# Kernel optimization log

Measured on AMD Instinct MI355X. Metric: run time of the kernel, lower is better.

Reference implementation:

```python
import jax, jax.numpy as jnp
import numpy as np

N, E, D, H, OUT = 100000, 1600000, 64, 64, 4


def _glorot(key, i, o):
    s = (6.0 / (i + o)) ** 0.5
    return jax.random.uniform(key, (i, o), jnp.float32, -s, s)


def setup_inputs() -> dict:
    key = jax.random.key(0)
    ks = jax.random.split(key, 5)
    x = jax.random.normal(ks[0], (N, D), jnp.float32)
    edge_index = jax.random.randint(ks[1], (2, E), 0, N, jnp.int32)
    return {
        "x": x,
        "edge_index": edge_index,
        "W0": _glorot(ks[2], D, H), "b0": jnp.zeros((H,), jnp.float32),
        "W1": _glorot(ks[3], H, H), "b1": jnp.zeros((H,), jnp.float32),
        "W2": _glorot(ks[4], H, OUT), "b2": jnp.zeros((OUT,), jnp.float32),
    }


def _gcn_layer(x, src, dst, W, b):
    # WeightedGCNConv.forward: remove_self_loops, then gcn_norm with
    # add_self_loops=True (self-loop weight 1), symmetric normalization,
    # scatter-add aggregation, then Linear.
    n = x.shape[0]
    w = (src != dst).astype(x.dtype)           # zero out original self loops
    deg = jax.ops.segment_sum(w, dst, num_segments=n) + 1.0  # +1 from added self loop
    dis = jax.lax.rsqrt(deg)                   # deg >= 1, no inf
    norm = dis[src] * w * dis[dst]             # [E]
    agg = jax.ops.segment_sum(norm[:, None] * x[src], dst, num_segments=n)
    agg = agg + (dis * dis)[:, None] * x       # self-loop contribution
    return agg @ W + b


def reference(x, edge_index, W0, b0, W1, b1, W2, b2):
    src, dst = edge_index[0], edge_index[1]    # flow source_to_target
    # Dropout is identity in eval mode.
    h = jax.nn.relu(_gcn_layer(x, src, dst, W0, b0))
    h = jax.nn.relu(_gcn_layer(h, src, dst, W1, b1))
    return _gcn_layer(h, src, dst, W2, b2)     # [N, 4]
```

## Files before the change

kernel.cpp:

```cpp
#include <hip/hip_runtime.h>
#include <hip/hip_fp16.h>


#define BLK 256
#define NBITS 7
#define NBW   (1 << NBITS)
#define G     8
#define CHUNK 4096
#define EPT   (CHUNK / BLK)
#define CAPG  384
#define PAD   16

__global__ void k_binA(const int* __restrict__ src, const int* __restrict__ dst,
                       int* __restrict__ bcur, int* __restrict__ binned,
                       int E, int nb) {
    __shared__ int lcnt[1024];
    __shared__ int lbase[1024];
    int t = threadIdx.x;
    int g = blockIdx.x & (G - 1);
    for (int i = t; i < nb; i += BLK) lcnt[i] = 0;
    __syncthreads();

    int e0 = blockIdx.x * CHUNK;
    int bs[EPT], vs[EPT];
#pragma unroll
    for (int i = 0; i < EPT; ++i) {
        int e = e0 + i * BLK + t;
        bs[i] = -1;
        if (e < E) {
            int s = src[e], d = dst[e];
            if (s != d) {
                bs[i] = d >> NBITS;
                vs[i] = (s << NBITS) | (d & (NBW - 1));
                atomicAdd(&lcnt[bs[i]], 1);
            }
        }
    }
    __syncthreads();
    for (int i = t; i < nb; i += BLK) {
        int c = lcnt[i];
        lbase[i] = c ? atomicAdd(&bcur[(g * nb + i) * PAD], c) : 0;
    }
    __syncthreads();
    for (int i = t; i < nb; i += BLK) lcnt[i] = 0;
    __syncthreads();
#pragma unroll
    for (int i = 0; i < EPT; ++i) {
        if (bs[i] >= 0) {
            int p = lbase[bs[i]] + atomicAdd(&lcnt[bs[i]], 1);
            if (p < CAPG) binned[(size_t)(g * nb + bs[i]) * CAPG + p] = vs[i];
        }
    }
}

__global__ void k_binB(const int* __restrict__ bcur, const int* __restrict__ binned,
                       int* __restrict__ cursor, int2* __restrict__ rowinfo,
                       float* __restrict__ dis, int* __restrict__ srcs,
                       int n, int nb) {
    __shared__ int cnt[NBW];
    __shared__ int scan[NBW];
    __shared__ int sbase;
    int b = blockIdx.x;
    int t = threadIdx.x;
    if (t < NBW) cnt[t] = 0;
    __syncthreads();
    for (int g = 0; g < G; ++g) {
        int m = min(bcur[(g * nb + b) * PAD], CAPG);
        const int* reg = binned + (size_t)(g * nb + b) * CAPG;
        for (int i = t; i < m; i += BLK)
            atomicAdd(&cnt[reg[i] & (NBW - 1)], 1);
    }
    __syncthreads();
    int c = 0;
    if (t < NBW) { c = cnt[t]; scan[t] = c; }
    __syncthreads();
    for (int off = 1; off < NBW; off <<= 1) {
        int u = (t < NBW && t >= off) ? scan[t - off] : 0;
        __syncthreads();
        if (t < NBW) scan[t] += u;
        __syncthreads();
    }
    if (t == NBW - 1) sbase = atomicAdd(cursor, scan[NBW - 1]);
    __syncthreads();
    int base = sbase;
    if (t < NBW) {
        int excl = scan[t] - c;
        int node = b * NBW + t;
        if (node < n) {
            rowinfo[node] = make_int2(base + excl, c);
            dis[node] = rsqrtf((float)c + 1.0f);
        }
    }
    __syncthreads();
    if (t < NBW) scan[t] = scan[t] - c;
    __syncthreads();
    for (int g = 0; g < G; ++g) {
        int m = min(bcur[(g * nb + b) * PAD], CAPG);
        const int* reg = binned + (size_t)(g * nb + b) * CAPG;
        for (int i = t; i < m; i += BLK) {
            int v = reg[i];
            int p = atomicAdd(&scan[v & (NBW - 1)], 1);
            srcs[base + p] = v >> NBITS;
        }
    }
}

__global__ void k_gemm64(const float* __restrict__ in, const float* __restrict__ W,
                         const float* __restrict__ dis, __half* __restrict__ z16, int n) {
    __shared__ float rows[4][64];
    int c  = threadIdx.x & 63;
    int r4 = threadIdx.x >> 6;
    float Wr[64];
#pragma unroll
    for (int k = 0; k < 64; ++k) Wr[k] = W[k * 64 + c];
    const float4* rp = reinterpret_cast<const float4*>(&rows[r4][0]);
    for (long base = (long)blockIdx.x * 4; base < n; base += (long)gridDim.x * 4) {
        long row = base + r4;
        __syncthreads();
        if (row < n) rows[r4][c] = in[row * 64 + c];
        __syncthreads();
        if (row < n) {
            float acc = 0.0f;
#pragma unroll
            for (int k4 = 0; k4 < 16; ++k4) {
                float4 rv = rp[k4];
                acc = fmaf(rv.x, Wr[4 * k4 + 0], acc);
                acc = fmaf(rv.y, Wr[4 * k4 + 1], acc);
                acc = fmaf(rv.z, Wr[4 * k4 + 2], acc);
                acc = fmaf(rv.w, Wr[4 * k4 + 3], acc);
            }
            z16[row * 64 + c] = __float2half(dis[row] * acc);
        }
    }
}

__device__ __forceinline__ float4 gather_row(const float2* __restrict__ zrow,
                                             const int2* __restrict__ rowinfo,
                                             const int* __restrict__ srcs,
                                             int node, int lane, int p, int hi) {
    float4 acc = make_float4(0.f, 0.f, 0.f, 0.f);
    if (hi == 0) {
        float2 r = zrow[(long)node * 16 + p];
        float2 a = __half22float2(*reinterpret_cast<__half2*>(&r.x));
        float2 bq = __half22float2(*reinterpret_cast<__half2*>(&r.y));
        acc = make_float4(a.x, a.y, bq.x, bq.y);
    }
    int2 ri = rowinfo[node];
    int beg = ri.x, end = ri.x + ri.y;
    for (int base = beg; base < end; base += 64) {
        int m = min(end - base, 64);
        int s = (lane < m) ? srcs[base + lane] : 0;
        int mf = m & ~3;
#pragma unroll 8
        for (int j = 0; j < mf; j += 4) {
            int sj = __shfl(s, j + hi);
            float2 r = zrow[(long)sj * 16 + p];
            float2 a = __half22float2(*reinterpret_cast<__half2*>(&r.x));
            float2 bq = __half22float2(*reinterpret_cast<__half2*>(&r.y));
            acc.x += a.x; acc.y += a.y; acc.z += bq.x; acc.w += bq.y;
        }
        if (m & 3) {
            int idx = mf + hi;
            int sj = __shfl(s, idx < 64 ? idx : 63);
            if (idx < m) {
                float2 r = zrow[(long)sj * 16 + p];
                float2 a = __half22float2(*reinterpret_cast<__half2*>(&r.x));
                float2 bq = __half22float2(*reinterpret_cast<__half2*>(&r.y));
                acc.x += a.x; acc.y += a.y; acc.z += bq.x; acc.w += bq.y;
            }
        }
    }
    acc.x += __shfl_xor(acc.x, 16); acc.y += __shfl_xor(acc.y, 16);
    acc.z += __shfl_xor(acc.z, 16); acc.w += __shfl_xor(acc.w, 16);
    acc.x += __shfl_xor(acc.x, 32); acc.y += __shfl_xor(acc.y, 32);
    acc.z += __shfl_xor(acc.z, 32); acc.w += __shfl_xor(acc.w, 32);
    return acc;
}

__global__ void k_aggW1(const float2* __restrict__ zrow, const int2* __restrict__ rowinfo,
                        const int* __restrict__ srcs, const float* __restrict__ dis,
                        const float* __restrict__ b0, const float* __restrict__ W1,
                        __half* __restrict__ z1, int n) {
    __shared__ __half2 W1t[32 * 64];
    __shared__ float hrow[4][64];
    for (int i = threadIdx.x; i < 32 * 64; i += BLK) {
        int c = i & 63, k2 = i >> 6;
        W1t[i] = __floats2half2_rn(W1[(2 * k2) * 64 + c], W1[(2 * k2 + 1) * 64 + c]);
    }
    __syncthreads();

    int lane = threadIdx.x & 63;
    int wv   = threadIdx.x >> 6;
    int node = blockIdx.x * (BLK / 64) + wv;
    if (node >= n) return;
    int p = lane & 15, hi = lane >> 4;

    float4 acc = gather_row(zrow, rowinfo, srcs, node, lane, p, hi);

    float dd = dis[node];
    float4 bb = reinterpret_cast<const float4*>(b0)[p];
    if (hi == 0) {
        float4 h;
        h.x = fmaxf(dd * acc.x + bb.x, 0.f);
        h.y = fmaxf(dd * acc.y + bb.y, 0.f);
        h.z = fmaxf(dd * acc.z + bb.z, 0.f);
        h.w = fmaxf(dd * acc.w + bb.w, 0.f);
        *reinterpret_cast<float4*>(&hrow[wv][4 * p]) = h;
    }
    asm volatile("s_waitcnt lgkmcnt(0)" ::: "memory");

    const float4* hq = reinterpret_cast<const float4*>(&hrow[wv][0]);
    float o = 0.f;
#pragma unroll
    for (int k4 = 0; k4 < 16; ++k4) {
        float4 hv = hq[k4];
        float2 wa = __half22float2(W1t[(2 * k4 + 0) * 64 + lane]);
        float2 wb = __half22float2(W1t[(2 * k4 + 1) * 64 + lane]);
        o = fmaf(hv.x, wa.x, o);
        o = fmaf(hv.y, wa.y, o);
        o = fmaf(hv.z, wb.x, o);
        o = fmaf(hv.w, wb.y, o);
    }
    z1[(long)node * 64 + lane] = __float2half(dd * o);
}

__global__ void k_aggW2(const float2* __restrict__ zrow, const int2* __restrict__ rowinfo,
                        const int* __restrict__ srcs, const float* __restrict__ dis,
                        const float* __restrict__ b1, const float* __restrict__ W2,
                        float* __restrict__ y2, int n) {
    __shared__ float W2l[64 * 4];
    if (threadIdx.x < 256) W2l[threadIdx.x] = W2[threadIdx.x];
    __syncthreads();
    int lane = threadIdx.x & 63;
    int node = blockIdx.x * (BLK / 64) + (threadIdx.x >> 6);
    if (node >= n) return;
    int p = lane & 15, hi = lane >> 4;

    float4 acc = gather_row(zrow, rowinfo, srcs, node, lane, p, hi);

    float dd = dis[node];
    float4 bb = reinterpret_cast<const float4*>(b1)[p];
    float h0 = fmaxf(dd * acc.x + bb.x, 0.f);
    float h1 = fmaxf(dd * acc.y + bb.y, 0.f);
    float h2 = fmaxf(dd * acc.z + bb.z, 0.f);
    float h3 = fmaxf(dd * acc.w + bb.w, 0.f);
    float pc[4];
#pragma unroll
    for (int c = 0; c < 4; ++c) {
        pc[c] = h0 * W2l[(4 * p + 0) * 4 + c] + h1 * W2l[(4 * p + 1) * 4 + c]
              + h2 * W2l[(4 * p + 2) * 4 + c] + h3 * W2l[(4 * p + 3) * 4 + c];
    }
#pragma unroll
    for (int off = 1; off < 16; off <<= 1) {
#pragma unroll
        for (int c = 0; c < 4; ++c) pc[c] += __shfl_xor(pc[c], off);
    }
    if (lane == 0) {
        reinterpret_cast<float4*>(y2)[node] =
            make_float4(dd * pc[0], dd * pc[1], dd * pc[2], dd * pc[3]);
    }
}

__global__ void k_agg4(const float* __restrict__ z2, const int2* __restrict__ rowinfo,
                       const int* __restrict__ srcs, const float* __restrict__ dis,
                       const float* __restrict__ b, float* __restrict__ out, int n) {
    long t = (long)blockIdx.x * blockDim.x + threadIdx.x;
    int i = (int)(t >> 2), c = (int)(t & 3);
    if (i < n) {
        float acc = z2[(long)i * 4 + c];
        int2 ri = rowinfo[i];
        int beg = ri.x, end = ri.x + ri.y;
        for (int e = beg; e < end; ++e)
            acc += z2[(long)srcs[e] * 4 + c];
        out[(long)i * 4 + c] = dis[i] * acc + b[c];
    }
}

extern "C" void kernel_launch(void* const* d_in, const int* in_sizes, int n_in,
                              void* d_out, int out_size, void* d_ws, size_t ws_size,
                              hipStream_t stream) {
    const float* x  = (const float*)d_in[0];
    const int*   ei = (const int*)d_in[1];
    const float* W0 = (const float*)d_in[2];
    const float* b0 = (const float*)d_in[3];
    const float* W1 = (const float*)d_in[4];
    const float* b1 = (const float*)d_in[5];
    const float* W2 = (const float*)d_in[6];
    const float* b2 = (const float*)d_in[7];
    float* out = (float*)d_out;

    const int n = in_sizes[0] / 64;
    const int E = in_sizes[1] / 2;
    const int* src = ei;
    const int* dst = ei + E;
    const int nb = (n + NBW - 1) / NBW;

    int*    bcur     = (int*)d_ws;
    int*    cursor   = bcur + G * nb * PAD;
    int2*   rowinfo  = (int2*)(cursor + 16);
    int*    srcs     = (int*)(rowinfo + n);
    float*  dis      = (float*)(srcs + E);
    __half* z16      = (__half*)(dis + n);
    __half* z1       = z16 + (size_t)n * 64;
    float*  y2       = (float*)(z1 + (size_t)n * 64);
    int*    binned   = (int*)z1;

    const int gWave  = (n + (BLK / 64) - 1) / (BLK / 64);
    const int gN4    = (int)(((long)n * 4 + BLK - 1) / BLK);
    const int gGemm  = 2048;
    const int nchunk = (E + CHUNK - 1) / CHUNK;

    hipMemsetAsync(bcur, 0, ((size_t)G * nb * PAD + 16) * sizeof(int), stream);
    k_binA<<<nchunk, BLK, 0, stream>>>(src, dst, bcur, binned, E, nb);
    k_binB<<<nb, BLK, 0, stream>>>(bcur, binned, cursor, rowinfo, dis, srcs, n, nb);

    k_gemm64<<<gGemm, BLK, 0, stream>>>(x, W0, dis, z16, n);

    k_aggW1<<<gWave, BLK, 0, stream>>>((const float2*)z16, rowinfo, srcs, dis, b0, W1,
                                       z1, n);

    k_aggW2<<<gWave, BLK, 0, stream>>>((const float2*)z1, rowinfo, srcs, dis, b1, W2,
                                       y2, n);

    k_agg4<<<gN4, BLK, 0, stream>>>(y2, rowinfo, srcs, dis, b2, out, n);
}
```

Before: 248.3 us.

## Unfuse layer-1 transform into separate aggregate and GEMM kernels; reread edges in binning

Splits the fused aggregate+W1 kernel into a pure aggregation kernel that writes the biased fp16 row, followed by a templated GEMM kernel that applies ReLU on load and scales by dis. The binning kernel now streams each chunk twice from global memory instead of holding edges in registers, and the chunk size is doubled. This is meant to cut register pressure and per-wave LDS work in the aggregation kernel. In exchange it adds an extra kernel launch, an extra fp16 round trip of the full hidden activation, and a second read of the edge list during binning.

```diff
diff --git a/kernel.cpp b/kernel.cpp
--- a/kernel.cpp
+++ b/kernel.cpp
@@ -6,8 +6,7 @@
 #define NBITS 7
 #define NBW   (1 << NBITS)
 #define G     8
-#define CHUNK 4096
-#define EPT   (CHUNK / BLK)
+#define CHUNK 8192
 #define CAPG  384
 #define PAD   16
 
@@ -22,33 +21,24 @@
     __syncthreads();
 
     int e0 = blockIdx.x * CHUNK;
-    int bs[EPT], vs[EPT];
-#pragma unroll
-    for (int i = 0; i < EPT; ++i) {
-        int e = e0 + i * BLK + t;
-        bs[i] = -1;
-        if (e < E) {
-            int s = src[e], d = dst[e];
-            if (s != d) {
-                bs[i] = d >> NBITS;
-                vs[i] = (s << NBITS) | (d & (NBW - 1));
-                atomicAdd(&lcnt[bs[i]], 1);
-            }
-        }
+    int e1 = min(e0 + CHUNK, E);
+    for (int e = e0 + t; e < e1; e += BLK) {
+        int s = src[e], d = dst[e];
+        if (s != d) atomicAdd(&lcnt[d >> NBITS], 1);
     }
     __syncthreads();
     for (int i = t; i < nb; i += BLK) {
         int c = lcnt[i];
         lbase[i] = c ? atomicAdd(&bcur[(g * nb + i) * PAD], c) : 0;
-    }
-    __syncthreads();
-    for (int i = t; i < nb; i += BLK) lcnt[i] = 0;
-    __syncthreads();
-#pragma unroll
-    for (int i = 0; i < EPT; ++i) {
-        if (bs[i] >= 0) {
-            int p = lbase[bs[i]] + atomicAdd(&lcnt[bs[i]], 1);
-            if (p < CAPG) binned[(size_t)(g * nb + bs[i]) * CAPG + p] = vs[i];
+        lcnt[i] = 0;
+    }
+    __syncthreads();
+    for (int e = e0 + t; e < e1; e += BLK) {
+        int s = src[e], d = dst[e];
+        if (s != d) {
+            int b = d >> NBITS;
+            int p = lbase[b] + atomicAdd(&lcnt[b], 1);
+            if (p < CAPG) binned[(size_t)(g * nb + b) * CAPG + p] = (s << NBITS) | (d & (NBW - 1));
         }
     }
 }
@@ -105,7 +95,11 @@
     }
 }
 
-__global__ void k_gemm64(const float* __restrict__ in, const float* __restrict__ W,
+__device__ __forceinline__ float ldf(const float* p, long i) { return p[i]; }
+__device__ __forceinline__ float ldf(const __half* p, long i) { return __half2float(p[i]); }
+
+template <bool RELU, typename TIN>
+__global__ void k_gemm64(const TIN* __restrict__ in, const float* __restrict__ W,
                          const float* __restrict__ dis, __half* __restrict__ z16, int n) {
     __shared__ float rows[4][64];
     int c  = threadIdx.x & 63;
@@ -117,7 +111,10 @@
     for (long base = (long)blockIdx.x * 4; base < n; base += (long)gridDim.x * 4) {
         long row = base + r4;
         __syncthreads();
-        if (row < n) rows[r4][c] = in[row * 64 + c];
+        if (row < n) {
+            float v = ldf(in, row * 64 + c);
+            rows[r4][c] = RELU ? fmaxf(v, 0.0f) : v;
+        }
         __syncthreads();
         if (row < n) {
             float acc = 0.0f;
@@ -177,51 +174,26 @@
     return acc;
 }
 
-__global__ void k_aggW1(const float2* __restrict__ zrow, const int2* __restrict__ rowinfo,
-                        const int* __restrict__ srcs, const float* __restrict__ dis,
-                        const float* __restrict__ b0, const float* __restrict__ W1,
-                        __half* __restrict__ z1, int n) {
-    __shared__ __half2 W1t[32 * 64];
-    __shared__ float hrow[4][64];
-    for (int i = threadIdx.x; i < 32 * 64; i += BLK) {
-        int c = i & 63, k2 = i >> 6;
-        W1t[i] = __floats2half2_rn(W1[(2 * k2) * 64 + c], W1[(2 * k2 + 1) * 64 + c]);
-    }
-    __syncthreads();
-
+__global__ void k_aggregate(const float2* __restrict__ zrow, const int2* __restrict__ rowinfo,
+                            const int* __restrict__ srcs, const float* __restrict__ dis,
+                            const float* __restrict__ bias, uint2* __restrict__ agg, int n) {
     int lane = threadIdx.x & 63;
-    int wv   = threadIdx.x >> 6;
-    int node = blockIdx.x * (BLK / 64) + wv;
+    int node = blockIdx.x * (BLK / 64) + (threadIdx.x >> 6);
     if (node >= n) return;
     int p = lane & 15, hi = lane >> 4;
 
     float4 acc = gather_row(zrow, rowinfo, srcs, node, lane, p, hi);
 
-    float dd = dis[node];
-    float4 bb = reinterpret_cast<const float4*>(b0)[p];
     if (hi == 0) {
-        float4 h;
-        h.x = fmaxf(dd * acc.x + bb.x, 0.f);
-        h.y = fmaxf(dd * acc.y + bb.y, 0.f);
-        h.z = fmaxf(dd * acc.z + bb.z, 0.f);
-        h.w = fmaxf(dd * acc.w + bb.w, 0.f);
-        *reinterpret_cast<float4*>(&hrow[wv][4 * p]) = h;
-    }
-    asm volatile("s_waitcnt lgkmcnt(0)" ::: "memory");
-
-    const float4* hq = reinterpret_cast<const float4*>(&hrow[wv][0]);
-    float o = 0.f;
-#pragma unroll
-    for (int k4 = 0; k4 < 16; ++k4) {
-        float4 hv = hq[k4];
-        float2 wa = __half22float2(W1t[(2 * k4 + 0) * 64 + lane]);
-        float2 wb = __half22float2(W1t[(2 * k4 + 1) * 64 + lane]);
-        o = fmaf(hv.x, wa.x, o);
-        o = fmaf(hv.y, wa.y, o);
-        o = fmaf(hv.z, wb.x, o);
-        o = fmaf(hv.w, wb.y, o);
-    }
-    z1[(long)node * 64 + lane] = __float2half(dd * o);
+        float dd = dis[node];
+        float4 bb = reinterpret_cast<const float4*>(bias)[p];
+        __half2 o0 = __floats2half2_rn(dd * acc.x + bb.x, dd * acc.y + bb.y);
+        __half2 o1 = __floats2half2_rn(dd * acc.z + bb.z, dd * acc.w + bb.w);
+        uint2 u;
+        u.x = *reinterpret_cast<unsigned int*>(&o0);
+        u.y = *reinterpret_cast<unsigned int*>(&o1);
+        agg[(long)node * 16 + p] = u;
+    }
 }
 
 __global__ void k_aggW2(const float2* __restrict__ zrow, const int2* __restrict__ rowinfo,
@@ -301,9 +273,9 @@
     int*    srcs     = (int*)(rowinfo + n);
     float*  dis      = (float*)(srcs + E);
     __half* z16      = (__half*)(dis + n);
-    __half* z1       = z16 + (size_t)n * 64;
-    float*  y2       = (float*)(z1 + (size_t)n * 64);
-    int*    binned   = (int*)z1;
+    __half* bufA     = z16 + (size_t)n * 64;
+    float*  y2       = (float*)(bufA + (size_t)n * 64);
+    int*    binned   = (int*)bufA;
 
     const int gWave  = (n + (BLK / 64) - 1) / (BLK / 64);
     const int gN4    = (int)(((long)n * 4 + BLK - 1) / BLK);
@@ -314,12 +286,12 @@
     k_binA<<<nchunk, BLK, 0, stream>>>(src, dst, bcur, binned, E, nb);
     k_binB<<<nb, BLK, 0, stream>>>(bcur, binned, cursor, rowinfo, dis, srcs, n, nb);
 
-    k_gemm64<<<gGemm, BLK, 0, stream>>>(x, W0, dis, z16, n);
-
-    k_aggW1<<<gWave, BLK, 0, stream>>>((const float2*)z16, rowinfo, srcs, dis, b0, W1,
-                                       z1, n);
-
-    k_aggW2<<<gWave, BLK, 0, stream>>>((const float2*)z1, rowinfo, srcs, dis, b1, W2,
+    k_gemm64<false, float><<<gGemm, BLK, 0, stream>>>(x, W0, dis, z16, n);
+    k_aggregate<<<gWave, BLK, 0, stream>>>((const float2*)z16, rowinfo, srcs, dis, b0,
+                                           (uint2*)bufA, n);
+
+    k_gemm64<true, __half><<<gGemm, BLK, 0, stream>>>(bufA, W1, dis, z16, n);
+    k_aggW2<<<gWave, BLK, 0, stream>>>((const float2*)z16, rowinfo, srcs, dis, b1, W2,
                                        y2, n);
 
     k_agg4<<<gN4, BLK, 0, stream>>>(y2, rowinfo, srcs, dis, b2, out, n);
```

After: 261.8 us. +5.4%, slower.
